# Kernel optimization log

Hardware: AMD Instinct MI355X
Metric: run time of the kernel (lower is better)

The kernel has to match this reference:

```python
import jax, jax.numpy as jnp
import numpy as np
from jax.ops import segment_sum, segment_max

N, E, P = 3072, 147456, 100000
IN_CH, HID, HEADS, LAYERS = 128, 256, 4, 2
WL, RWSE_DIM = 16, 16
DH = HID // HEADS


def setup_inputs() -> dict:
    key = jax.random.key(0)
    ks = jax.random.split(key, 16)
    s = 0.05
    return {
        "x": jax.random.normal(ks[0], (N, IN_CH), jnp.float32),
        "edge_index": jax.random.randint(ks[1], (2, E), 0, N, jnp.int32),
        "src": jax.random.randint(ks[2], (P,), 0, N, jnp.int32),
        "dst": jax.random.randint(ks[3], (P,), 0, N, jnp.int32),
        "rwse_w": jax.random.normal(ks[4], (WL, RWSE_DIM), jnp.float32) * s,
        "rwse_b": jnp.zeros((RWSE_DIM,), jnp.float32),
        "proj_w": jax.random.normal(ks[5], (IN_CH + RWSE_DIM, HID), jnp.float32) * s,
        "proj_b": jnp.zeros((HID,), jnp.float32),
        "Wq": jax.random.normal(ks[6], (LAYERS, HID, HID), jnp.float32) * s,
        "bq": jnp.zeros((LAYERS, HID), jnp.float32),
        "Wk": jax.random.normal(ks[7], (LAYERS, HID, HID), jnp.float32) * s,
        "bk": jnp.zeros((LAYERS, HID), jnp.float32),
        "Wv": jax.random.normal(ks[8], (LAYERS, HID, HID), jnp.float32) * s,
        "bv": jnp.zeros((LAYERS, HID), jnp.float32),
        "Ws": jax.random.normal(ks[9], (LAYERS, HID, HID), jnp.float32) * s,
        "bs": jnp.zeros((LAYERS, HID), jnp.float32),
        "ln_g": jnp.ones((LAYERS, HID), jnp.float32),
        "ln_b": jnp.zeros((LAYERS, HID), jnp.float32),
    }


def _layernorm(h, g, b):
    mu = h.mean(-1, keepdims=True)
    var = ((h - mu) ** 2).mean(-1, keepdims=True)
    return (h - mu) * jax.lax.rsqrt(var + 1e-5) * g + b


def reference(x, edge_index, src, dst, rwse_w, rwse_b, proj_w, proj_b,
              Wq, bq, Wk, bk, Wv, bv, Ws, bs, ln_g, ln_b):
    n = x.shape[0]
    # --- RWSE positional encoding (dense random-walk diagonals) ---
    adj = jnp.zeros((n, n), x.dtype).at[edge_index[0], edge_index[1]].add(1.0)
    deg = jnp.clip(adj.sum(axis=1, keepdims=True), 1.0, None)
    rw = adj / deg  # row-normalized transition matrix

    def step(power, _):
        power = power @ rw
        return power, jnp.diagonal(power)

    _, diags = jax.lax.scan(step, jnp.eye(n, dtype=x.dtype), None, length=WL)
    pe = diags.T @ rwse_w + rwse_b  # [n, RWSE_DIM]

    # --- input projection ---
    h = jnp.concatenate([x, pe], axis=-1) @ proj_w + proj_b  # [n, HID]

    sidx, tidx = edge_index[0], edge_index[1]  # message j -> i (source, target)
    scale = 1.0 / np.sqrt(DH)
    for l in range(LAYERS):
        q = (h @ Wq[l] + bq[l]).reshape(n, HEADS, DH)
        k = (h @ Wk[l] + bk[l]).reshape(n, HEADS, DH)
        v = (h @ Wv[l] + bv[l]).reshape(n, HEADS, DH)
        # per-edge attention logits [E, HEADS]
        score = (q[tidx] * k[sidx]).sum(-1) * scale
        # segment softmax over incoming edges of each target node
        m = segment_max(score, tidx, num_segments=n)
        m = jnp.where(jnp.isfinite(m), m, 0.0)
        e = jnp.exp(score - m[tidx])
        denom = segment_sum(e, tidx, num_segments=n)
        alpha = e / jnp.maximum(denom[tidx], 1e-16)
        agg = segment_sum(alpha[:, :, None] * v[sidx], tidx, num_segments=n)
        out = agg.reshape(n, HID) + h @ Ws[l] + bs[l]  # attn + root skip (lin_skip)
        h = jax.nn.relu(_layernorm(h + out, ln_g[l], ln_b[l]))

    # --- dot-product link decode ---
    return jax.nn.sigmoid((h[src] * h[dst]).sum(-1))
```

## Files before the change

kernel.cpp:

```cpp
#include <hip/hip_runtime.h>
#include <hip/hip_bf16.h>
#include <hip/hip_fp8.h>

#define NN   3072
#define NE   147456
#define NP   100000
#define HID  256
#define INCH 128
#define CATK 144
#define KPAD 160
#define FP8_S    1024.0f
#define FP8_IS   (1.0f / 1024.0f)
#define FP8_IS2  (1.0f / (1024.0f * 1024.0f))
#define MAXE 128

typedef __attribute__((ext_vector_type(4))) float    f32x4;
typedef __attribute__((ext_vector_type(8))) _Float16 f16x8;
typedef __attribute__((ext_vector_type(4))) _Float16 f16x4;
typedef __attribute__((ext_vector_type(8))) unsigned char u8x8;
typedef __attribute__((ext_vector_type(4))) int i32x4;
typedef __attribute__((ext_vector_type(8))) int i32x8;

__device__ __forceinline__ float fp8f(unsigned char b) {
  __hip_fp8_e4m3 t; t.__x = b; return (float)t;
}
__device__ __forceinline__ unsigned char f2fp8(float v) {
  __hip_fp8_e4m3 t(v); return t.__x;
}

__device__ __forceinline__ void gload16(const void* g, void* l) {
  __builtin_amdgcn_global_load_lds((const __attribute__((address_space(1))) void*)g,
                                   (__attribute__((address_space(3))) void*)l, 16, 0, 0);
}

__global__ void edges_kernel(const int* __restrict__ ei, float* __restrict__ adj,
                             int* __restrict__ cnt) {
  int e = blockIdx.x * 256 + threadIdx.x;
  if (e < NE) {
    int s = ei[e], t = ei[NE + e];
    atomicAdd(&adj[(size_t)s * NN + t], 1.0f);
    atomicAdd(&cnt[t], 1);
  }
}

__global__ void rownorm_kernel(const float* __restrict__ adj, unsigned char* __restrict__ rw,
                               float* __restrict__ diag1) {
  int row = blockIdx.x, tid = threadIdx.x;
  const float* ap = adj + (size_t)row * NN;
  float s = 0.f;
  for (int j = tid; j < NN; j += 256) s += ap[j];
  for (int d = 32; d; d >>= 1) s += __shfl_xor(s, d);
  __shared__ float w4[4];
  if ((tid & 63) == 0) w4[tid >> 6] = s;
  __syncthreads();
  float inv = 1.f / fmaxf(w4[0] + w4[1] + w4[2] + w4[3], 1.f);
  unsigned char* rp = rw + (size_t)row * NN;
  for (int j = tid; j < NN; j += 256) {
    float v = ap[j] * inv;
    rp[j] = f2fp8(v * FP8_S);
    if (j == row) diag1[row] = v;
  }
}

__global__ void transpose2_u8_kernel(const unsigned char* __restrict__ in0,
                                     unsigned char* __restrict__ out0,
                                     const unsigned char* __restrict__ in1,
                                     unsigned char* __restrict__ out1) {
  const unsigned char* in = blockIdx.z ? in1 : in0;
  unsigned char* out = blockIdx.z ? out1 : out0;
  __shared__ unsigned char t[64][68];
  int bx = blockIdx.x, by = blockIdx.y, tid = threadIdx.x;
#pragma unroll
  for (int ii = 0; ii < 4; ii++) {
    int lin = ii * 256 + tid;
    int r = lin >> 4, c4 = (lin & 15) * 4;
    unsigned int v = *(const unsigned int*)(in + (size_t)(by * 64 + r) * NN + bx * 64 + c4);
    t[r][c4] = v & 255; t[r][c4 + 1] = (v >> 8) & 255;
    t[r][c4 + 2] = (v >> 16) & 255; t[r][c4 + 3] = v >> 24;
  }
  __syncthreads();
#pragma unroll
  for (int ii = 0; ii < 4; ii++) {
    int lin = ii * 256 + tid;
    int r = lin >> 4, c4 = (lin & 15) * 4;
    unsigned int v = (unsigned int)t[c4][r] | ((unsigned int)t[c4 + 1][r] << 8) |
                     ((unsigned int)t[c4 + 2][r] << 16) | ((unsigned int)t[c4 + 3][r] << 24);
    *(unsigned int*)(out + (size_t)(bx * 64 + r) * NN + by * 64 + c4) = v;
  }
}

__global__ __launch_bounds__(256) void gemm_fp8_nt(const unsigned char* __restrict__ A,
                                                   const unsigned char* __restrict__ Bt,
                                                   unsigned char* __restrict__ C, int n) {
  __shared__ __align__(16) unsigned char As[128 * 128];
  __shared__ __align__(16) unsigned char Bs[128 * 128];
  const int nbx = n >> 7;
  const int nb = nbx * nbx;
  const int bid = blockIdx.x;
  const int cpx = nb >> 3;
  const int wg = (bid & 7) * cpx + (bid >> 3);
  const int by = wg / nbx, bx = wg % nbx;
  const int tid = threadIdx.x;
  const int lane = tid & 63, wave = tid >> 6;
  const int wr = wave >> 1, wc = wave & 1;
  const int rowA0 = by * 128, rowB0 = bx * 128;
  const int fr = lane & 15;
  const int kg = lane >> 4;
  const int sr = tid >> 3;
  const int scd = tid & 7;
  f32x4 acc[4][4] = {};
  const int nkt = n >> 7;
  for (int kt = 0; kt < nkt; ++kt) {
    const int k0 = kt << 7;
#pragma unroll
    for (int s = 0; s < 4; s++) {
      const int row = sr + s * 32;
      const int cg = (scd ^ (row & 7)) << 4;
      gload16(A + (size_t)(rowA0 + row) * n + k0 + cg, As + row * 128 + scd * 16);
      gload16(Bt + (size_t)(rowB0 + row) * n + k0 + cg, Bs + row * 128 + scd * 16);
    }
    __syncthreads();
    i32x8 af[4], bf[4];
#pragma unroll
    for (int i = 0; i < 4; i++) {
      const int Ra = wr * 64 + i * 16 + fr;
      const int Rb = wc * 64 + i * 16 + fr;
      const int c0a = ((2 * kg) ^ (Ra & 7)) << 4, c1a = ((2 * kg + 1) ^ (Ra & 7)) << 4;
      const int c0b = ((2 * kg) ^ (Rb & 7)) << 4, c1b = ((2 * kg + 1) ^ (Rb & 7)) << 4;
      i32x4 alo = *(const i32x4*)(As + Ra * 128 + c0a);
      i32x4 ahi = *(const i32x4*)(As + Ra * 128 + c1a);
      i32x4 blo = *(const i32x4*)(Bs + Rb * 128 + c0b);
      i32x4 bhi = *(const i32x4*)(Bs + Rb * 128 + c1b);
      af[i] = (i32x8){alo[0], alo[1], alo[2], alo[3], ahi[0], ahi[1], ahi[2], ahi[3]};
      bf[i] = (i32x8){blo[0], blo[1], blo[2], blo[3], bhi[0], bhi[1], bhi[2], bhi[3]};
    }
#pragma unroll
    for (int i = 0; i < 4; i++)
#pragma unroll
      for (int j = 0; j < 4; j++)
        acc[i][j] = __builtin_amdgcn_mfma_scale_f32_16x16x128_f8f6f4(
            af[i], bf[j], acc[i][j], 0, 0, 0, 127, 0, 127);
    __syncthreads();
  }
  const int crow0 = rowA0 + wr * 64, ccol0 = rowB0 + wc * 64;
#pragma unroll
  for (int i = 0; i < 4; i++)
#pragma unroll
    for (int j = 0; j < 4; j++)
#pragma unroll
      for (int r = 0; r < 4; r++) {
        int row = crow0 + i * 16 + (lane >> 4) * 4 + r;
        int col = ccol0 + j * 16 + (lane & 15);
        C[(size_t)row * n + col] = f2fp8(acc[i][j][r] * FP8_IS);
      }
}

__global__ __launch_bounds__(256) void diag_all_kernel(
    const unsigned char* __restrict__ rw, const unsigned char* __restrict__ rw2,
    const unsigned char* __restrict__ rw4, const unsigned char* __restrict__ rw8,
    const unsigned char* __restrict__ rw12, const unsigned char* __restrict__ rwT,
    const unsigned char* __restrict__ rw2T, const unsigned char* __restrict__ rw3T,
    const unsigned char* __restrict__ rw4T, float* __restrict__ diags) {
  int row = blockIdx.x, tid = threadIdx.x;
  size_t base = (size_t)row * NN;
  const u8x8* pl1  = (const u8x8*)(rw + base);
  const u8x8* pl2  = (const u8x8*)(rw2 + base);
  const u8x8* pl4  = (const u8x8*)(rw4 + base);
  const u8x8* pl8  = (const u8x8*)(rw8 + base);
  const u8x8* pl12 = (const u8x8*)(rw12 + base);
  const u8x8* pr1  = (const u8x8*)(rwT + base);
  const u8x8* pr2  = (const u8x8*)(rw2T + base);
  const u8x8* pr3  = (const u8x8*)(rw3T + base);
  const u8x8* pr4  = (const u8x8*)(rw4T + base);
  float s[15];
#pragma unroll
  for (int k = 0; k < 15; k++) s[k] = 0.f;
  for (int j = tid; j < NN / 8; j += 256) {
    u8x8 L1 = pl1[j], L2 = pl2[j], L4 = pl4[j], L8 = pl8[j], L12 = pl12[j];
    u8x8 R1 = pr1[j], R2 = pr2[j], R3 = pr3[j], R4 = pr4[j];
#pragma unroll
    for (int r = 0; r < 8; r++) {
      float a1 = fp8f(L1[r]), a2 = fp8f(L2[r]), a4 = fp8f(L4[r]),
            a8 = fp8f(L8[r]), a12 = fp8f(L12[r]);
      float b1 = fp8f(R1[r]), b2 = fp8f(R2[r]), b3 = fp8f(R3[r]), b4 = fp8f(R4[r]);
      s[0]  += a1 * b1;  s[1]  += a2 * b1;  s[2]  += a2 * b2;
      s[3]  += a4 * b1;  s[4]  += a4 * b2;  s[5]  += a4 * b3;  s[6]  += a4 * b4;
      s[7]  += a8 * b1;  s[8]  += a8 * b2;  s[9]  += a8 * b3;  s[10] += a8 * b4;
      s[11] += a12 * b1; s[12] += a12 * b2; s[13] += a12 * b3; s[14] += a12 * b4;
    }
  }
  __shared__ float red[15][4];
  int wave = tid >> 6, lane = tid & 63;
#pragma unroll
  for (int k = 0; k < 15; k++) {
    float v = s[k];
    for (int d = 32; d; d >>= 1) v += __shfl_xor(v, d);
    if (lane == 0) red[k][wave] = v;
  }
  __syncthreads();
  if (tid < 15)
    diags[(size_t)(tid + 1) * NN + row] =
        (red[tid][0] + red[tid][1] + red[tid][2] + red[tid][3]) * FP8_IS2;
}

__global__ __launch_bounds__(256) void gemm_f16_node(const _Float16* __restrict__ A,
                                                     const _Float16* __restrict__ Bt,
                                                     const float* __restrict__ bias,
                                                     const float* __restrict__ addhi,
                                                     float* __restrict__ C32,
                                                     _Float16* __restrict__ C16,
                                                     int M, int Nn, int K) {
  __shared__ _Float16 As[64 * 32];
  __shared__ _Float16 Bs[64 * 32];
  const int tid = threadIdx.x;
  const int lane = tid & 63, wave = tid >> 6;
  const int wr = wave >> 1, wc = wave & 1;
  const int m0 = blockIdx.y * 64, n0 = blockIdx.x * 64;
  const int fr = lane & 15, fk = (lane >> 4) * 8;
  const int gr = tid >> 2, gc = (tid & 3) * 8;
  f32x4 acc[2][2] = {};
  for (int k0 = 0; k0 < K; k0 += 32) {
    gload16(A + (size_t)(m0 + gr) * K + k0 + gc, As + tid * 8);
    gload16(Bt + (size_t)(n0 + gr) * K + k0 + gc, Bs + tid * 8);
    __syncthreads();
    f16x8 af[2], bf[2];
#pragma unroll
    for (int i = 0; i < 2; i++) {
      af[i] = *(const f16x8*)(As + (wr * 32 + i * 16 + fr) * 32 + fk);
      bf[i] = *(const f16x8*)(Bs + (wc * 32 + i * 16 + fr) * 32 + fk);
    }
#pragma unroll
    for (int i = 0; i < 2; i++)
#pragma unroll
      for (int j = 0; j < 2; j++)
        acc[i][j] = __builtin_amdgcn_mfma_f32_16x16x32_f16(af[i], bf[j], acc[i][j], 0, 0, 0);
    __syncthreads();
  }
  const int crow0 = m0 + wr * 32, ccol0 = n0 + wc * 32;
#pragma unroll
  for (int i = 0; i < 2; i++)
#pragma unroll
    for (int j = 0; j < 2; j++)
#pragma unroll
      for (int r = 0; r < 4; r++) {
        int row = crow0 + i * 16 + (lane >> 4) * 4 + r;
        int col = ccol0 + j * 16 + (lane & 15);
        float val = acc[i][j][r];
        if (bias) val += bias[col];
        if (addhi && col >= Nn - 256) val += addhi[(size_t)row * 256 + col - (Nn - 256)];
        if (C32) C32[(size_t)row * Nn + col] = val;
        if (C16) C16[(size_t)row * Nn + col] = (_Float16)val;
      }
}

__global__ void wconv_proj_kernel(const float* __restrict__ W, _Float16* __restrict__ Wt) {
  int idx = blockIdx.x * 256 + threadIdx.x;
  if (idx >= HID * KPAD) return;
  int n = idx / KPAD, k = idx - n * KPAD;
  Wt[idx] = (k < CATK) ? (_Float16)W[(size_t)k * HID + n] : (_Float16)0.f;
}

__global__ void wconv_cat_kernel(const float* __restrict__ Wq, const float* __restrict__ Wk,
                                 const float* __restrict__ Wv, const float* __restrict__ Wsk,
                                 const float* __restrict__ bq, const float* __restrict__ bk,
                                 const float* __restrict__ bv, const float* __restrict__ bsk,
                                 _Float16* __restrict__ wt, float* __restrict__ bcat) {
  int idx = blockIdx.x * 256 + threadIdx.x;
  if (idx < 1024) {
    int s = idx >> 8, j = idx & 255;
    bcat[idx] = (s == 0) ? bq[j] : (s == 1) ? bk[j] : (s == 2) ? bv[j] : bsk[j];
  }
  if (idx < 4 * HID * HID) {
    int nrow = idx >> 8, k = idx & 255;
    int s = nrow >> 8, nc = nrow & 255;
    const float* W = (s == 0) ? Wq : (s == 1) ? Wk : (s == 2) ? Wv : Wsk;
    wt[idx] = (_Float16)W[(size_t)k * HID + nc];
  }
}

__global__ void concat16_kernel(const float* __restrict__ x, const float* __restrict__ diags,
                                const float* __restrict__ w, const float* __restrict__ bb,
                                _Float16* __restrict__ xc) {
  int idx = blockIdx.x * 256 + threadIdx.x;
  if (idx >= NN * KPAD) return;
  int i = idx / KPAD, c = idx - i * KPAD;
  float v;
  if (c < INCH) v = x[(size_t)i * INCH + c];
  else if (c < CATK) {
    int d = c - INCH;
    v = bb[d];
#pragma unroll
    for (int t = 0; t < 16; t++) v += diags[t * NN + i] * w[t * 16 + d];
  } else v = 0.f;
  xc[idx] = (_Float16)v;
}

__global__ void csr_scan_kernel(const int* __restrict__ cnt, int* __restrict__ off) {
  int lane = threadIdx.x;
  const int per = NN / 64;
  int s = 0;
  for (int i = 0; i < per; i++) s += cnt[lane * per + i];
  int run = s;
  for (int d = 1; d < 64; d <<= 1) {
    int t = __shfl_up(run, d);
    if (lane >= d) run += t;
  }
  int acc = run - s;
  for (int i = 0; i < per; i++) {
    off[lane * per + i] = acc;
    acc += cnt[lane * per + i];
  }
  if (lane == 63) off[NN] = acc;
}

__global__ void csr_fill_kernel(const int* __restrict__ sidx, const int* __restrict__ tidx,
                                const int* __restrict__ off, int* __restrict__ cur,
                                int* __restrict__ csrc) {
  int e = blockIdx.x * 256 + threadIdx.x;
  if (e >= NE) return;
  int t = tidx[e];
  int pos = atomicAdd(&cur[t], 1);
  csrc[off[t] + pos] = sidx[e];
}

__global__ __launch_bounds__(256) void attn_ln_kernel(const int* __restrict__ off,
                                                      const int* __restrict__ csrc,
                                                      const _Float16* __restrict__ qkvz,
                                                      const float* __restrict__ g,
                                                      const float* __restrict__ b,
                                                      float* __restrict__ hb,
                                                      _Float16* __restrict__ h16) {
  int node = blockIdx.x, tid = threadIdx.x;
  int h = tid >> 6, lane = tid & 63;
  int beg = off[node], end = off[node + 1];
  __shared__ _Float16 qs[256];
  __shared__ int srcs[MAXE];
  __shared__ float ps[4][MAXE];
  qs[tid] = qkvz[(size_t)node * 1024 + tid];
  float m_run = -INFINITY, d_run = 0.f, acc = 0.f;
  for (int chunk = beg; chunk < end; chunk += MAXE) {
    int ne = min(end - chunk, MAXE);
    if (tid < ne) srcs[tid] = csrc[chunk + tid];
    __syncthreads();
    for (int p = tid; p < ne * 4; p += 256) {
      int e = p >> 2, h2 = p & 3;
      const f16x8* krow = (const f16x8*)(qkvz + (size_t)srcs[e] * 1024 + 256 + h2 * 64);
      const f16x8* qrow = (const f16x8*)(qs + h2 * 64);
      float sc = 0.f;
#pragma unroll
      for (int d8 = 0; d8 < 8; d8++) {
        f16x8 kv = krow[d8], qv = qrow[d8];
#pragma unroll
        for (int r = 0; r < 8; r++) sc += (float)qv[r] * (float)kv[r];
      }
      ps[h2][e] = sc * 0.125f;
    }
    __syncthreads();
    float mloc = -INFINITY;
    for (int e = lane; e < ne; e += 64) mloc = fmaxf(mloc, ps[h][e]);
    for (int d = 32; d; d >>= 1) mloc = fmaxf(mloc, __shfl_xor(mloc, d));
    float mnew = fmaxf(m_run, mloc);
    float dloc = 0.f;
    for (int e = lane; e < ne; e += 64) {
      float p = __expf(ps[h][e] - mnew);
      ps[h][e] = p;
      dloc += p;
    }
    for (int d = 32; d; d >>= 1) dloc += __shfl_xor(dloc, d);
    float scale = __expf(m_run - mnew);
    d_run = d_run * scale + dloc;
    acc *= scale;
    for (int e = 0; e < ne; e++) {
      acc += ps[h][e] * (float)qkvz[(size_t)srcs[e] * 1024 + 512 + h * 64 + lane];
    }
    m_run = mnew;
    __syncthreads();
  }
  float agg = acc / fmaxf(d_run, 1e-16f);
  float z = (float)qkvz[(size_t)node * 1024 + 768 + tid] + agg;
  float s = z;
  for (int d = 32; d; d >>= 1) s += __shfl_xor(s, d);
  __shared__ float w4[4], w4b[4];
  if (lane == 0) w4[h] = s;
  __syncthreads();
  float mu = (w4[0] + w4[1] + w4[2] + w4[3]) * (1.f / HID);
  float dv = z - mu;
  float qv = dv * dv;
  for (int d = 32; d; d >>= 1) qv += __shfl_xor(qv, d);
  if (lane == 0) w4b[h] = qv;
  __syncthreads();
  float var = (w4b[0] + w4b[1] + w4b[2] + w4b[3]) * (1.f / HID);
  float y = dv * (1.f / sqrtf(var + 1e-5f)) * g[tid] + b[tid];
  y = fmaxf(y, 0.f);
  hb[(size_t)node * HID + tid] = y;
  h16[(size_t)node * HID + tid] = (_Float16)y;
}

__global__ void decode_kernel(const _Float16* __restrict__ h, const int* __restrict__ src,
                              const int* __restrict__ dst, float* __restrict__ out) {
  int wv = threadIdx.x >> 6, lane = threadIdx.x & 63;
  int p = blockIdx.x * 4 + wv;
  if (p >= NP) return;
  const f16x4* a = (const f16x4*)(h + (size_t)src[p] * HID);
  const f16x4* b = (const f16x4*)(h + (size_t)dst[p] * HID);
  f16x4 x = a[lane], y = b[lane];
  float s = (float)x[0] * (float)y[0] + (float)x[1] * (float)y[1] +
            (float)x[2] * (float)y[2] + (float)x[3] * (float)y[3];
  for (int d = 32; d; d >>= 1) s += __shfl_xor(s, d);
  if (lane == 0) out[p] = 1.f / (1.f + expf(-s));
}

extern "C" void kernel_launch(void* const* d_in, const int* in_sizes, int n_in,
                              void* d_out, int out_size, void* d_ws, size_t ws_size,
                              hipStream_t stream) {
  const float* x      = (const float*)d_in[0];
  const int*   ei     = (const int*)d_in[1];
  const int*   src    = (const int*)d_in[2];
  const int*   dst    = (const int*)d_in[3];
  const float* rwse_w = (const float*)d_in[4];
  const float* rwse_b = (const float*)d_in[5];
  const float* proj_w = (const float*)d_in[6];
  const float* proj_b = (const float*)d_in[7];
  const float* Wq     = (const float*)d_in[8];
  const float* bq     = (const float*)d_in[9];
  const float* Wk     = (const float*)d_in[10];
  const float* bk     = (const float*)d_in[11];
  const float* Wv     = (const float*)d_in[12];
  const float* bv     = (const float*)d_in[13];
  const float* Wsk    = (const float*)d_in[14];
  const float* bs     = (const float*)d_in[15];
  const float* ln_g   = (const float*)d_in[16];
  const float* ln_b   = (const float*)d_in[17];
  float* out = (float*)d_out;

  const size_t M8 = (size_t)NN * NN;
  char* base = (char*)d_ws;
  unsigned char* rw   = (unsigned char*)(base + 0 * M8);
  unsigned char* rwT  = (unsigned char*)(base + 1 * M8);
  unsigned char* rw2  = (unsigned char*)(base + 2 * M8);
  unsigned char* rw3  = (unsigned char*)(base + 3 * M8);
  unsigned char* rw4  = (unsigned char*)(base + 4 * M8);
  unsigned char* rw4T = (unsigned char*)(base + 5 * M8);
  unsigned char* rw8  = (unsigned char*)(base + 6 * M8);
  unsigned char* rw12 = (unsigned char*)(base + 7 * M8);
  unsigned char* rw2T = (unsigned char*)(base + 8 * M8);
  unsigned char* rw3T = (unsigned char*)(base + 9 * M8);
  float* adj = (float*)(base + 6 * M8);
  char* sm = base + 10 * M8;
  float* diags = (float*)sm; sm += (size_t)16 * NN * 4;
  int* cnt = (int*)sm; sm += 12288;
  int* cur = (int*)sm; sm += 12288;
  int* off = (int*)sm; sm += 16384;
  int* csrc = (int*)sm; sm += (size_t)NE * 4;
  float* hbuf = (float*)sm; sm += (size_t)NN * HID * 4;
  _Float16* qkvz16 = (_Float16*)sm; sm += (size_t)NN * 1024 * 2;
  _Float16* h16  = (_Float16*)sm; sm += (size_t)NN * HID * 2;
  _Float16* xc16 = (_Float16*)sm; sm += (size_t)NN * KPAD * 2;
  _Float16* wt_proj = (_Float16*)sm; sm += (size_t)HID * KPAD * 2;
  _Float16* wt_cat[2]; float* bcat[2];
  for (int l = 0; l < 2; ++l) {
    wt_cat[l] = (_Float16*)sm; sm += (size_t)4 * HID * HID * 2;
    bcat[l]   = (float*)sm;    sm += 1024 * 4;
  }
  (void)in_sizes; (void)n_in; (void)out_size; (void)ws_size;

  const dim3 B256(256);
  const dim3 gT1(NN / 64, NN / 64, 1);
  const dim3 gT2(NN / 64, NN / 64, 2);
  const int  gG = (NN / 128) * (NN / 128);
  const dim3 gW(1024 / 64, NN / 64);
  const dim3 gS(HID / 64, NN / 64);

  wconv_proj_kernel<<<(HID * KPAD + 255) / 256, B256, 0, stream>>>(proj_w, wt_proj);
  for (int l = 0; l < 2; ++l)
    wconv_cat_kernel<<<(4 * HID * HID + 255) / 256, B256, 0, stream>>>(
        Wq + (size_t)l * HID * HID, Wk + (size_t)l * HID * HID, Wv + (size_t)l * HID * HID,
        Wsk + (size_t)l * HID * HID, bq + l * HID, bk + l * HID, bv + l * HID, bs + l * HID,
        wt_cat[l], bcat[l]);

  hipMemsetAsync(adj, 0, (size_t)NN * NN * 4, stream);
  hipMemsetAsync(cnt, 0, 24576, stream);
  edges_kernel<<<(NE + 255) / 256, B256, 0, stream>>>(ei, adj, cnt);
  rownorm_kernel<<<NN, B256, 0, stream>>>(adj, rw, diags);
  csr_scan_kernel<<<1, 64, 0, stream>>>(cnt, off);
  csr_fill_kernel<<<(NE + 255) / 256, B256, 0, stream>>>(ei, ei + NE, off, cur, csrc);

  transpose2_u8_kernel<<<gT1, B256, 0, stream>>>(rw, rwT, rw, rwT);
  gemm_fp8_nt<<<gG, B256, 0, stream>>>(rw, rwT, rw2, NN);
  gemm_fp8_nt<<<gG, B256, 0, stream>>>(rw2, rwT, rw3, NN);
  gemm_fp8_nt<<<gG, B256, 0, stream>>>(rw3, rwT, rw4, NN);
  transpose2_u8_kernel<<<gT1, B256, 0, stream>>>(rw4, rw4T, rw4, rw4T);
  gemm_fp8_nt<<<gG, B256, 0, stream>>>(rw4, rw4T, rw8, NN);
  gemm_fp8_nt<<<gG, B256, 0, stream>>>(rw8, rw4T, rw12, NN);
  transpose2_u8_kernel<<<gT2, B256, 0, stream>>>(rw2, rw2T, rw3, rw3T);
  diag_all_kernel<<<NN, B256, 0, stream>>>(rw, rw2, rw4, rw8, rw12,
                                           rwT, rw2T, rw3T, rw4T, diags);

  concat16_kernel<<<(NN * KPAD + 255) / 256, B256, 0, stream>>>(x, diags, rwse_w, rwse_b, xc16);
  gemm_f16_node<<<gS, B256, 0, stream>>>(xc16, wt_proj, proj_b, nullptr, hbuf, h16,
                                         NN, HID, KPAD);

  for (int l = 0; l < 2; ++l) {
    gemm_f16_node<<<gW, B256, 0, stream>>>(h16, wt_cat[l], bcat[l], hbuf, nullptr, qkvz16,
                                           NN, 1024, HID);
    attn_ln_kernel<<<NN, B256, 0, stream>>>(off, csrc, qkvz16, ln_g + l * HID, ln_b + l * HID,
                                            hbuf, h16);
  }

  decode_kernel<<<NP / 4, B256, 0, stream>>>(h16, src, dst, out);
}
```

Baseline: 520.2 us.

## Merge prep kernels, drop fp32 hidden buffer, unroll value gather

Folds the weight conversions, edge scatter, row normalisation, CSR scan/fill and the transposes into fewer multi-role launches, cutting launch count and serialization. It also drops the fp32 hidden-state buffer: the skip path now reads the fp16 copy and attention no longer writes fp32. The value aggregation loop in attention is unrolled by four so more gathers are in flight at once. The fp16 skip input adds some rounding error to the residual path.

```diff
diff --git a/kernel.cpp b/kernel.cpp
--- a/kernel.cpp
+++ b/kernel.cpp
@@ -33,43 +33,97 @@
                                    (__attribute__((address_space(3))) void*)l, 16, 0, 0);
 }
 
-__global__ void edges_kernel(const int* __restrict__ ei, float* __restrict__ adj,
-                             int* __restrict__ cnt) {
-  int e = blockIdx.x * 256 + threadIdx.x;
-  if (e < NE) {
-    int s = ei[e], t = ei[NE + e];
-    atomicAdd(&adj[(size_t)s * NN + t], 1.0f);
-    atomicAdd(&cnt[t], 1);
-  }
-}
-
-__global__ void rownorm_kernel(const float* __restrict__ adj, unsigned char* __restrict__ rw,
-                               float* __restrict__ diag1) {
-  int row = blockIdx.x, tid = threadIdx.x;
-  const float* ap = adj + (size_t)row * NN;
-  float s = 0.f;
-  for (int j = tid; j < NN; j += 256) s += ap[j];
-  for (int d = 32; d; d >>= 1) s += __shfl_xor(s, d);
-  __shared__ float w4[4];
-  if ((tid & 63) == 0) w4[tid >> 6] = s;
-  __syncthreads();
-  float inv = 1.f / fmaxf(w4[0] + w4[1] + w4[2] + w4[3], 1.f);
-  unsigned char* rp = rw + (size_t)row * NN;
-  for (int j = tid; j < NN; j += 256) {
-    float v = ap[j] * inv;
-    rp[j] = f2fp8(v * FP8_S);
-    if (j == row) diag1[row] = v;
-  }
-}
-
-__global__ void transpose2_u8_kernel(const unsigned char* __restrict__ in0,
-                                     unsigned char* __restrict__ out0,
-                                     const unsigned char* __restrict__ in1,
-                                     unsigned char* __restrict__ out1) {
-  const unsigned char* in = blockIdx.z ? in1 : in0;
-  unsigned char* out = blockIdx.z ? out1 : out0;
+__global__ void prep_kernel(const int* __restrict__ ei, float* __restrict__ adj,
+                            int* __restrict__ cnt,
+                            const float* __restrict__ proj_w, _Float16* __restrict__ wt_proj,
+                            const float* __restrict__ Wq, const float* __restrict__ Wk,
+                            const float* __restrict__ Wv, const float* __restrict__ Wsk,
+                            const float* __restrict__ bq, const float* __restrict__ bk,
+                            const float* __restrict__ bv, const float* __restrict__ bsk,
+                            _Float16* __restrict__ wt_cat0, _Float16* __restrict__ wt_cat1,
+                            float* __restrict__ bcat0, float* __restrict__ bcat1) {
+  int bid = blockIdx.x, tid = threadIdx.x;
+  if (bid < 576) {
+    int e = bid * 256 + tid;
+    if (e < NE) {
+      int s = ei[e], t = ei[NE + e];
+      atomicAdd(&adj[(size_t)s * NN + t], 1.0f);
+      atomicAdd(&cnt[t], 1);
+    }
+    return;
+  }
+  if (bid < 736) {
+    int idx = (bid - 576) * 256 + tid;
+    if (idx < HID * KPAD) {
+      int n = idx / KPAD, k = idx - n * KPAD;
+      wt_proj[idx] = (k < CATK) ? (_Float16)proj_w[(size_t)k * HID + n] : (_Float16)0.f;
+    }
+    return;
+  }
+  int l = (bid < 1760) ? 0 : 1;
+  int idx = (bid - (l ? 1760 : 736)) * 256 + tid;
+  const float* Wq_ = Wq + (size_t)l * HID * HID;
+  const float* Wk_ = Wk + (size_t)l * HID * HID;
+  const float* Wv_ = Wv + (size_t)l * HID * HID;
+  const float* Ws_ = Wsk + (size_t)l * HID * HID;
+  _Float16* wt = l ? wt_cat1 : wt_cat0;
+  float* bcat = l ? bcat1 : bcat0;
+  if (idx < 1024) {
+    int s = idx >> 8, j = idx & 255;
+    bcat[idx] = (s == 0) ? bq[l * HID + j] : (s == 1) ? bk[l * HID + j]
+              : (s == 2) ? bv[l * HID + j] : bsk[l * HID + j];
+  }
+  if (idx < 4 * HID * HID) {
+    int nrow = idx >> 8, k = idx & 255;
+    int s = nrow >> 8, nc = nrow & 255;
+    const float* W = (s == 0) ? Wq_ : (s == 1) ? Wk_ : (s == 2) ? Wv_ : Ws_;
+    wt[idx] = (_Float16)W[(size_t)k * HID + nc];
+  }
+}
+
+__global__ void rownorm_scan_kernel(const float* __restrict__ adj, unsigned char* __restrict__ rw,
+                                    float* __restrict__ diag1,
+                                    const int* __restrict__ cnt, int* __restrict__ off) {
+  int bid = blockIdx.x, tid = threadIdx.x;
+  if (bid < NN) {
+    const float* ap = adj + (size_t)bid * NN;
+    float s = 0.f;
+    for (int j = tid; j < NN; j += 256) s += ap[j];
+    for (int d = 32; d; d >>= 1) s += __shfl_xor(s, d);
+    __shared__ float w4[4];
+    if ((tid & 63) == 0) w4[tid >> 6] = s;
+    __syncthreads();
+    float inv = 1.f / fmaxf(w4[0] + w4[1] + w4[2] + w4[3], 1.f);
+    unsigned char* rp = rw + (size_t)bid * NN;
+    for (int j = tid; j < NN; j += 256) {
+      float v = ap[j] * inv;
+      rp[j] = f2fp8(v * FP8_S);
+      if (j == bid) diag1[bid] = v;
+    }
+    return;
+  }
+  if (tid >= 64) return;
+  int lane = tid;
+  const int per = NN / 64;
+  int s = 0;
+  for (int i = 0; i < per; i++) s += cnt[lane * per + i];
+  int run = s;
+  for (int d = 1; d < 64; d <<= 1) {
+    int t = __shfl_up(run, d);
+    if (lane >= d) run += t;
+  }
+  int acc = run - s;
+  for (int i = 0; i < per; i++) {
+    off[lane * per + i] = acc;
+    acc += cnt[lane * per + i];
+  }
+  if (lane == 63) off[NN] = acc;
+}
+
+__device__ __forceinline__ void transpose_body(const unsigned char* __restrict__ in,
+                                               unsigned char* __restrict__ out,
+                                               int bx, int by, int tid) {
   __shared__ unsigned char t[64][68];
-  int bx = blockIdx.x, by = blockIdx.y, tid = threadIdx.x;
 #pragma unroll
   for (int ii = 0; ii < 4; ii++) {
     int lin = ii * 256 + tid;
@@ -87,6 +141,33 @@
                      ((unsigned int)t[c4 + 2][r] << 16) | ((unsigned int)t[c4 + 3][r] << 24);
     *(unsigned int*)(out + (size_t)(bx * 64 + r) * NN + by * 64 + c4) = v;
   }
+}
+
+__global__ void fill_transpose_kernel(const int* __restrict__ sidx, const int* __restrict__ tidx,
+                                      const int* __restrict__ off, int* __restrict__ cur,
+                                      int* __restrict__ csrc,
+                                      const unsigned char* __restrict__ rw,
+                                      unsigned char* __restrict__ rwT) {
+  int bid = blockIdx.x, tid = threadIdx.x;
+  if (bid < 576) {
+    int e = bid * 256 + tid;
+    if (e < NE) {
+      int t = tidx[e];
+      int pos = atomicAdd(&cur[t], 1);
+      csrc[off[t] + pos] = sidx[e];
+    }
+    return;
+  }
+  int t = bid - 576;
+  transpose_body(rw, rwT, t % 48, t / 48, tid);
+}
+
+__global__ void transpose3_kernel(const unsigned char* __restrict__ rw4, unsigned char* __restrict__ rw4T,
+                                  const unsigned char* __restrict__ rw2, unsigned char* __restrict__ rw2T,
+                                  const unsigned char* __restrict__ rw3, unsigned char* __restrict__ rw3T) {
+  const unsigned char* in  = (blockIdx.z == 0) ? rw4  : (blockIdx.z == 1) ? rw2  : rw3;
+  unsigned char* out       = (blockIdx.z == 0) ? rw4T : (blockIdx.z == 1) ? rw2T : rw3T;
+  transpose_body(in, out, blockIdx.x, blockIdx.y, threadIdx.x);
 }
 
 __global__ __launch_bounds__(256) void gemm_fp8_nt(const unsigned char* __restrict__ A,
@@ -206,8 +287,7 @@
 __global__ __launch_bounds__(256) void gemm_f16_node(const _Float16* __restrict__ A,
                                                      const _Float16* __restrict__ Bt,
                                                      const float* __restrict__ bias,
-                                                     const float* __restrict__ addhi,
-                                                     float* __restrict__ C32,
+                                                     const _Float16* __restrict__ addhi,
                                                      _Float16* __restrict__ C16,
                                                      int M, int Nn, int K) {
   __shared__ _Float16 As[64 * 32];
@@ -247,35 +327,9 @@
         int col = ccol0 + j * 16 + (lane & 15);
         float val = acc[i][j][r];
         if (bias) val += bias[col];
-        if (addhi && col >= Nn - 256) val += addhi[(size_t)row * 256 + col - (Nn - 256)];
-        if (C32) C32[(size_t)row * Nn + col] = val;
-        if (C16) C16[(size_t)row * Nn + col] = (_Float16)val;
+        if (addhi && col >= Nn - 256) val += (float)addhi[(size_t)row * 256 + col - (Nn - 256)];
+        C16[(size_t)row * Nn + col] = (_Float16)val;
       }
-}
-
-__global__ void wconv_proj_kernel(const float* __restrict__ W, _Float16* __restrict__ Wt) {
-  int idx = blockIdx.x * 256 + threadIdx.x;
-  if (idx >= HID * KPAD) return;
-  int n = idx / KPAD, k = idx - n * KPAD;
-  Wt[idx] = (k < CATK) ? (_Float16)W[(size_t)k * HID + n] : (_Float16)0.f;
-}
-
-__global__ void wconv_cat_kernel(const float* __restrict__ Wq, const float* __restrict__ Wk,
-                                 const float* __restrict__ Wv, const float* __restrict__ Wsk,
-                                 const float* __restrict__ bq, const float* __restrict__ bk,
-                                 const float* __restrict__ bv, const float* __restrict__ bsk,
-                                 _Float16* __restrict__ wt, float* __restrict__ bcat) {
-  int idx = blockIdx.x * 256 + threadIdx.x;
-  if (idx < 1024) {
-    int s = idx >> 8, j = idx & 255;
-    bcat[idx] = (s == 0) ? bq[j] : (s == 1) ? bk[j] : (s == 2) ? bv[j] : bsk[j];
-  }
-  if (idx < 4 * HID * HID) {
-    int nrow = idx >> 8, k = idx & 255;
-    int s = nrow >> 8, nc = nrow & 255;
-    const float* W = (s == 0) ? Wq : (s == 1) ? Wk : (s == 2) ? Wv : Wsk;
-    wt[idx] = (_Float16)W[(size_t)k * HID + nc];
-  }
 }
 
 __global__ void concat16_kernel(const float* __restrict__ x, const float* __restrict__ diags,
@@ -295,40 +349,11 @@
   xc[idx] = (_Float16)v;
 }
 
-__global__ void csr_scan_kernel(const int* __restrict__ cnt, int* __restrict__ off) {
-  int lane = threadIdx.x;
-  const int per = NN / 64;
-  int s = 0;
-  for (int i = 0; i < per; i++) s += cnt[lane * per + i];
-  int run = s;
-  for (int d = 1; d < 64; d <<= 1) {
-    int t = __shfl_up(run, d);
-    if (lane >= d) run += t;
-  }
-  int acc = run - s;
-  for (int i = 0; i < per; i++) {
-    off[lane * per + i] = acc;
-    acc += cnt[lane * per + i];
-  }
-  if (lane == 63) off[NN] = acc;
-}
-
-__global__ void csr_fill_kernel(const int* __restrict__ sidx, const int* __restrict__ tidx,
-                                const int* __restrict__ off, int* __restrict__ cur,
-                                int* __restrict__ csrc) {
-  int e = blockIdx.x * 256 + threadIdx.x;
-  if (e >= NE) return;
-  int t = tidx[e];
-  int pos = atomicAdd(&cur[t], 1);
-  csrc[off[t] + pos] = sidx[e];
-}
-
 __global__ __launch_bounds__(256) void attn_ln_kernel(const int* __restrict__ off,
                                                       const int* __restrict__ csrc,
                                                       const _Float16* __restrict__ qkvz,
                                                       const float* __restrict__ g,
                                                       const float* __restrict__ b,
-                                                      float* __restrict__ hb,
                                                       _Float16* __restrict__ h16) {
   int node = blockIdx.x, tid = threadIdx.x;
   int h = tid >> 6, lane = tid & 63;
@@ -370,9 +395,17 @@
     float scale = __expf(m_run - mnew);
     d_run = d_run * scale + dloc;
     acc *= scale;
-    for (int e = 0; e < ne; e++) {
-      acc += ps[h][e] * (float)qkvz[(size_t)srcs[e] * 1024 + 512 + h * 64 + lane];
-    }
+    const size_t vb = 512 + (size_t)h * 64 + lane;
+    int e = 0;
+    for (; e + 4 <= ne; e += 4) {
+      float v0 = (float)qkvz[(size_t)srcs[e]     * 1024 + vb];
+      float v1 = (float)qkvz[(size_t)srcs[e + 1] * 1024 + vb];
+      float v2 = (float)qkvz[(size_t)srcs[e + 2] * 1024 + vb];
+      float v3 = (float)qkvz[(size_t)srcs[e + 3] * 1024 + vb];
+      acc += ps[h][e] * v0 + ps[h][e + 1] * v1 + ps[h][e + 2] * v2 + ps[h][e + 3] * v3;
+    }
+    for (; e < ne; ++e)
+      acc += ps[h][e] * (float)qkvz[(size_t)srcs[e] * 1024 + vb];
     m_run = mnew;
     __syncthreads();
   }
@@ -392,7 +425,6 @@
   float var = (w4b[0] + w4b[1] + w4b[2] + w4b[3]) * (1.f / HID);
   float y = dv * (1.f / sqrtf(var + 1e-5f)) * g[tid] + b[tid];
   y = fmaxf(y, 0.f);
-  hb[(size_t)node * HID + tid] = y;
   h16[(size_t)node * HID + tid] = (_Float16)y;
 }
 
@@ -452,7 +484,6 @@
   int* cur = (int*)sm; sm += 12288;
   int* off = (int*)sm; sm += 16384;
   int* csrc = (int*)sm; sm += (size_t)NE * 4;
-  float* hbuf = (float*)sm; sm += (size_t)NN * HID * 4;
   _Float16* qkvz16 = (_Float16*)sm; sm += (size_t)NN * 1024 * 2;
   _Float16* h16  = (_Float16*)sm; sm += (size_t)NN * HID * 2;
   _Float16* xc16 = (_Float16*)sm; sm += (size_t)NN * KPAD * 2;
@@ -465,46 +496,37 @@
   (void)in_sizes; (void)n_in; (void)out_size; (void)ws_size;
 
   const dim3 B256(256);
-  const dim3 gT1(NN / 64, NN / 64, 1);
-  const dim3 gT2(NN / 64, NN / 64, 2);
+  const dim3 gT3(NN / 64, NN / 64, 3);
   const int  gG = (NN / 128) * (NN / 128);
   const dim3 gW(1024 / 64, NN / 64);
   const dim3 gS(HID / 64, NN / 64);
 
-  wconv_proj_kernel<<<(HID * KPAD + 255) / 256, B256, 0, stream>>>(proj_w, wt_proj);
-  for (int l = 0; l < 2; ++l)
-    wconv_cat_kernel<<<(4 * HID * HID + 255) / 256, B256, 0, stream>>>(
-        Wq + (size_t)l * HID * HID, Wk + (size_t)l * HID * HID, Wv + (size_t)l * HID * HID,
-        Wsk + (size_t)l * HID * HID, bq + l * HID, bk + l * HID, bv + l * HID, bs + l * HID,
-        wt_cat[l], bcat[l]);
-
   hipMemsetAsync(adj, 0, (size_t)NN * NN * 4, stream);
   hipMemsetAsync(cnt, 0, 24576, stream);
-  edges_kernel<<<(NE + 255) / 256, B256, 0, stream>>>(ei, adj, cnt);
-  rownorm_kernel<<<NN, B256, 0, stream>>>(adj, rw, diags);
-  csr_scan_kernel<<<1, 64, 0, stream>>>(cnt, off);
-  csr_fill_kernel<<<(NE + 255) / 256, B256, 0, stream>>>(ei, ei + NE, off, cur, csrc);
-
-  transpose2_u8_kernel<<<gT1, B256, 0, stream>>>(rw, rwT, rw, rwT);
+
+  prep_kernel<<<2784, B256, 0, stream>>>(ei, adj, cnt, proj_w, wt_proj,
+                                         Wq, Wk, Wv, Wsk, bq, bk, bv, bs,
+                                         wt_cat[0], wt_cat[1], bcat[0], bcat[1]);
+  rownorm_scan_kernel<<<NN + 1, B256, 0, stream>>>(adj, rw, diags, cnt, off);
+  fill_transpose_kernel<<<576 + 2304, B256, 0, stream>>>(ei, ei + NE, off, cur, csrc, rw, rwT);
+
   gemm_fp8_nt<<<gG, B256, 0, stream>>>(rw, rwT, rw2, NN);
   gemm_fp8_nt<<<gG, B256, 0, stream>>>(rw2, rwT, rw3, NN);
   gemm_fp8_nt<<<gG, B256, 0, stream>>>(rw3, rwT, rw4, NN);
-  transpose2_u8_kernel<<<gT1, B256, 0, stream>>>(rw4, rw4T, rw4, rw4T);
+  transpose3_kernel<<<gT3, B256, 0, stream>>>(rw4, rw4T, rw2, rw2T, rw3, rw3T);
   gemm_fp8_nt<<<gG, B256, 0, stream>>>(rw4, rw4T, rw8, NN);
   gemm_fp8_nt<<<gG, B256, 0, stream>>>(rw8, rw4T, rw12, NN);
-  transpose2_u8_kernel<<<gT2, B256, 0, stream>>>(rw2, rw2T, rw3, rw3T);
   diag_all_kernel<<<NN, B256, 0, stream>>>(rw, rw2, rw4, rw8, rw12,
                                            rwT, rw2T, rw3T, rw4T, diags);
 
   concat16_kernel<<<(NN * KPAD + 255) / 256, B256, 0, stream>>>(x, diags, rwse_w, rwse_b, xc16);
-  gemm_f16_node<<<gS, B256, 0, stream>>>(xc16, wt_proj, proj_b, nullptr, hbuf, h16,
-                                         NN, HID, KPAD);
+  gemm_f16_node<<<gS, B256, 0, stream>>>(xc16, wt_proj, proj_b, nullptr, h16, NN, HID, KPAD);
 
   for (int l = 0; l < 2; ++l) {
-    gemm_f16_node<<<gW, B256, 0, stream>>>(h16, wt_cat[l], bcat[l], hbuf, nullptr, qkvz16,
+    gemm_f16_node<<<gW, B256, 0, stream>>>(h16, wt_cat[l], bcat[l], h16, qkvz16,
                                            NN, 1024, HID);
     attn_ln_kernel<<<NN, B256, 0, stream>>>(off, csrc, qkvz16, ln_g + l * HID, ln_b + l * HID,
-                                            hbuf, h16);
+                                            h16);
   }
 
   decode_kernel<<<NP / 4, B256, 0, stream>>>(h16, src, dst, out);
```

New measurement: 500.8 us. -3.7%, faster.
